# Optimization experiments

Measured on AMD Instinct MI355X. Metric: run time of the kernel, lower is better.

## Reference

```python
import jax, jax.numpy as jnp
import numpy as np

N_NODES = 25000
N_EDGES = 400000
HIDDEN = 256
NUM_FILTERS = 256
NUM_GAUSSIANS = 50
CUTOFF = 10.0


def ssp(x):
    # ShiftedSoftplus: softplus(x) - log(2)
    return jax.nn.softplus(x) - jnp.log(2.0).astype(x.dtype)


def setup_inputs() -> dict:
    key = jax.random.key(0)
    ks = jax.random.split(key, 12)
    s = 0.05
    return {
        "h": jax.random.normal(ks[0], (N_NODES, HIDDEN), dtype=jnp.float32),
        "pos": jax.random.uniform(ks[1], (N_NODES, 3), dtype=jnp.float32) * CUTOFF,
        "lin1_w": jax.random.normal(ks[2], (HIDDEN, NUM_FILTERS), dtype=jnp.float32) * s,
        "lin2_w": jax.random.normal(ks[3], (NUM_FILTERS, HIDDEN), dtype=jnp.float32) * s,
        "lin2_b": jnp.zeros((HIDDEN,), dtype=jnp.float32),
        "mlp_w1": jax.random.normal(ks[4], (NUM_GAUSSIANS, NUM_FILTERS), dtype=jnp.float32) * s,
        "mlp_b1": jnp.zeros((NUM_FILTERS,), dtype=jnp.float32),
        "mlp_w2": jax.random.normal(ks[5], (NUM_FILTERS, NUM_FILTERS), dtype=jnp.float32) * s,
        "mlp_b2": jnp.zeros((NUM_FILTERS,), dtype=jnp.float32),
        "lin_w": jax.random.normal(ks[6], (HIDDEN, HIDDEN), dtype=jnp.float32) * s,
        "lin_b": jnp.zeros((HIDDEN,), dtype=jnp.float32),
        "edge_index": jax.random.randint(ks[7], (2, N_EDGES), 0, N_NODES, dtype=jnp.int32),
    }


def reference(h, pos, lin1_w, lin2_w, lin2_b, mlp_w1, mlp_b1, mlp_w2, mlp_b2,
              lin_w, lin_b, edge_index):
    row, col = edge_index[0], edge_index[1]  # source, target (PyG convention)

    # edge distances
    diff = pos[row] - pos[col]                       # [E, 3]
    edge_weight = jnp.linalg.norm(diff, axis=-1)     # [E]

    # GaussianSmearing(0, cutoff, num_gaussians)
    offset = jnp.linspace(0.0, CUTOFF, NUM_GAUSSIANS, dtype=h.dtype)
    coeff = -0.5 / (offset[1] - offset[0]) ** 2
    edge_attr = jnp.exp(coeff * (edge_weight[:, None] - offset) ** 2)  # [E, G]

    # CFConv filter network * cosine cutoff
    W = ssp(edge_attr @ mlp_w1 + mlp_b1) @ mlp_w2 + mlp_b2             # [E, F]
    C = 0.5 * (jnp.cos(edge_weight * (jnp.pi / CUTOFF)) + 1.0)         # [E]
    W = W * C[:, None]

    # gather - multiply - scatter-add
    x = h @ lin1_w                                                     # [N, F] (no bias)
    msg = x[row] * W                                                   # [E, F]
    agg = jax.ops.segment_sum(msg, col, num_segments=N_NODES)          # [N, F]

    x = agg @ lin2_w + lin2_b
    x = ssp(x)
    h_update = x @ lin_w + lin_b                                       # [N, H]
    return (h_update, pos)
```

## Files before the change

### kernel.cpp

```cpp
#include <hip/hip_runtime.h>
#include <hip/hip_bf16.h>

#define N_NODES 25000
#define N_EDGES 400000
#define NTILES (N_EDGES / 32)

typedef __attribute__((ext_vector_type(8))) __bf16 bf16x8;
typedef __attribute__((ext_vector_type(4))) float f32x4;
typedef __attribute__((ext_vector_type(2))) unsigned uint32x2;

#define BAR() do {                                          \
    asm volatile("s_waitcnt lgkmcnt(0)" ::: "memory");      \
    __builtin_amdgcn_s_barrier();                           \
    asm volatile("" ::: "memory");                          \
} while (0)

static __device__ __forceinline__ unsigned short bfbits(float f) {
    __bf16 h = (__bf16)f;
    return __builtin_bit_cast(unsigned short, h);
}
static __device__ __forceinline__ float ssp_f(float x) {
    const float t = __builtin_amdgcn_exp2f(x * 1.44269504f);
    return 0.69314718f * (__builtin_amdgcn_logf(1.f + t) - 1.f);
}

template<int EPI, int OBF, int ABF>
__global__ __launch_bounds__(256, 2)
void node_gemm(const void* __restrict__ Av, const float* __restrict__ B,
               const float* __restrict__ bias, void* __restrict__ outv, int M)
{
    extern __shared__ char lds[];
    const int tid  = threadIdx.x;
    const int half = blockIdx.x & 1;
    const int jblk = half << 7;
    const int row0 = (blockIdx.x >> 1) << 7;

    {
        const int j   = tid & 127;
        const int k2b = (tid >> 7) << 6;
        for (int i = 0; i < 64; ++i) {
            const int k = (k2b + i) * 2;
            const float b0 = B[k * 256 + jblk + j];
            const float b1 = B[(k + 1) * 256 + jblk + j];
            const unsigned pack = (unsigned)bfbits(b0) | ((unsigned)bfbits(b1) << 16);
            *(unsigned*)(lds + ((j * 512 + k * 2) ^ ((j & 7) << 4))) = pack;
        }
    }
    __syncthreads();

    const int wave = tid >> 6;
    const int l    = tid & 63;
    const int lrow = l & 15;
    const int kg   = (l >> 4) << 3;

    f32x4 acc[8][2];
    const f32x4 z4 = {0.f, 0.f, 0.f, 0.f};
    #pragma unroll
    for (int m = 0; m < 8; ++m) { acc[m][0] = z4; acc[m][1] = z4; }

    #pragma unroll
    for (int ks = 0; ks < 8; ++ks) {
        const int k0 = (ks << 5) + kg;
        bf16x8 bfr[2];
        #pragma unroll
        for (int n = 0; n < 2; ++n) {
            const int jl = (wave << 5) + (n << 4) + lrow;
            bfr[n] = *(const bf16x8*)(lds + ((jl * 512 + k0 * 2) ^ ((jl & 7) << 4)));
        }
        #pragma unroll
        for (int m = 0; m < 8; ++m) {
            const int row = row0 + (m << 4) + lrow;
            bf16x8 af;
            if (row < M) {
                if (ABF) {
                    af = *(const bf16x8*)((const __bf16*)Av + row * 256 + k0);
                } else {
                    const float* ap = (const float*)Av + row * 256 + k0;
                    const f32x4 a0 = *(const f32x4*)(ap);
                    const f32x4 a1 = *(const f32x4*)(ap + 4);
                    #pragma unroll
                    for (int b = 0; b < 4; ++b) { af[b] = (__bf16)a0[b]; af[b + 4] = (__bf16)a1[b]; }
                }
            } else {
                #pragma unroll
                for (int b = 0; b < 8; ++b) af[b] = (__bf16)0.f;
            }
            acc[m][0] = __builtin_amdgcn_mfma_f32_16x16x32_bf16(af, bfr[0], acc[m][0], 0, 0, 0);
            acc[m][1] = __builtin_amdgcn_mfma_f32_16x16x32_bf16(af, bfr[1], acc[m][1], 0, 0, 0);
        }
    }

    #pragma unroll
    for (int m = 0; m < 8; ++m) {
        #pragma unroll
        for (int n = 0; n < 2; ++n) {
            const int j = jblk + (wave << 5) + (n << 4) + lrow;
            float bv = 0.f;
            if (EPI) bv = bias[j];
            #pragma unroll
            for (int r = 0; r < 4; ++r) {
                const int row = row0 + (m << 4) + ((l >> 4) << 2) + r;
                if (row < M) {
                    float v = acc[m][n][r] + bv;
                    if (EPI == 1) v = ssp_f(v);
                    if (OBF) ((unsigned short*)outv)[row * 256 + j] = bfbits(v);
                    else     ((float*)outv)[row * 256 + j] = v;
                }
            }
        }
    }
}

__global__ void hist_kernel(const int* __restrict__ ei, int* __restrict__ hist)
{
    const int i = blockIdx.x * 256 + threadIdx.x;
    if (i < N_EDGES) atomicAdd(&hist[ei[N_EDGES + i]], 1);
}

__global__ void scan_kernel(int* __restrict__ hist)
{
    __shared__ int part[1024];
    const int t  = threadIdx.x;
    const int CH = (N_NODES + 1023) / 1024;
    const int lo = t * CH;
    const int hi = (lo + CH < N_NODES) ? lo + CH : N_NODES;
    int s = 0;
    for (int i = lo; i < hi; ++i) s += hist[i];
    part[t] = s;
    __syncthreads();
    for (int off = 1; off < 1024; off <<= 1) {
        const int v = part[t];
        const int u = (t >= off) ? part[t - off] : 0;
        __syncthreads();
        part[t] = v + u;
        __syncthreads();
    }
    int base = (t == 0) ? 0 : part[t - 1];
    for (int i = lo; i < hi; ++i) { const int v = hist[i]; hist[i] = base; base += v; }
}

__global__ void scatter_meta(const int* __restrict__ ei, const float* __restrict__ pos,
                             int* __restrict__ hist, float4* __restrict__ meta,
                             float* __restrict__ out_pos)
{
    const int i = blockIdx.x * 256 + threadIdx.x;
    if (i >= N_EDGES) return;
    if (i < N_NODES * 3) out_pos[i] = pos[i];
    const int r = ei[i];
    const int c = ei[N_EDGES + i];
    const float dx = pos[r * 3 + 0] - pos[c * 3 + 0];
    const float dy = pos[r * 3 + 1] - pos[c * 3 + 1];
    const float dz = pos[r * 3 + 2] - pos[c * 3 + 2];
    const float d  = __fsqrt_rn(dx * dx + dy * dy + dz * dz);
    const float C  = 0.5f * (__cosf(d * 0.31415926535f) + 1.f);
    const int p = atomicAdd(&hist[c], 1);
    float4 m;
    m.x = d; m.y = C;
    m.z = __int_as_float(r); m.w = __int_as_float(c);
    meta[p] = m;
}

__global__ __launch_bounds__(256, 2)
void edge_kernel(const float4* __restrict__ meta,
                 const float* __restrict__ w1, const float* __restrict__ b1,
                 const float* __restrict__ w2, const float* __restrict__ b2,
                 const float* __restrict__ x, float* __restrict__ agg)
{
    extern __shared__ char lds[];
    char* w2t = lds;
    char* rb  = lds + 65536;
    int* colsm = (int*)(rb + 8192);

    const int tid   = threadIdx.x;
    const int wave  = tid >> 6;
    const int l     = tid & 63;
    const int lrow  = l & 15;
    const int g     = l >> 4;
    const int kg    = g << 3;
    const int half  = blockIdx.x & 1;
    const int jblk  = half << 7;
    const int group = blockIdx.x >> 1;

    {
        const int j   = tid & 127;
        const int k2b = (tid >> 7) << 6;
        for (int i = 0; i < 64; ++i) {
            const int k = (k2b + i) * 2;
            const float v0 = w2[k * 256 + jblk + j];
            const float v1 = w2[(k + 1) * 256 + jblk + j];
            const unsigned pack = (unsigned)bfbits(v0) | ((unsigned)bfbits(v1) << 16);
            *(unsigned*)(w2t + ((j * 512 + k * 2) ^ ((j & 7) << 4))) = pack;
        }
    }

    const float dlt    = 10.f / 49.f;
    const float coeff2 = (-0.5f / (dlt * dlt)) * 1.44269504f;
    bf16x8 w1f[4][2];
    #pragma unroll
    for (int n = 0; n < 4; ++n)
        #pragma unroll
        for (int ks = 0; ks < 2; ++ks) {
            bf16x8 v;
            #pragma unroll
            for (int b = 0; b < 8; ++b) {
                const int k = (ks << 5) + kg + b;
                const int j = (wave << 6) + (n << 4) + lrow;
                v[b] = (k < 50) ? (__bf16)w1[k * 256 + j] : (__bf16)0.f;
            }
            w1f[n][ks] = v;
        }
    float b1v[4], b2v[2];
    #pragma unroll
    for (int n = 0; n < 4; ++n) b1v[n] = b1[(wave << 6) + (n << 4) + lrow];
    #pragma unroll
    for (int n = 0; n < 2; ++n) b2v[n] = b2[jblk + (wave << 5) + (n << 4) + lrow];

    BAR();

    const f32x4 z4 = {0.f, 0.f, 0.f, 0.f};
    const int CH = (NTILES + 255) / 256;
    const int t0 = group * CH;
    int t1 = t0 + CH; if (t1 > NTILES) t1 = NTILES;

    const int ge  = tid >> 3;
    const int gkb = (tid & 7) << 3;

    int   rprev  = -1;
    float rs     = 0.f;
    int   rfirst = 1;
    float* aj    = agg + jblk + (tid & 127);

    for (int t = t0; t < t1; ++t) {
        const float4 mv = meta[(t << 5) + (l & 31)];
        const float d  = mv.x;
        const float Cc = mv.y;
        const int   r  = __float_as_int(mv.z);
        const int   c  = __float_as_int(mv.w);

        float xv[2][2][4];
        #pragma unroll
        for (int m = 0; m < 2; ++m)
            #pragma unroll
            for (int r4 = 0; r4 < 4; ++r4) {
                const int e  = (m << 4) + (g << 2) + r4;
                const int re = __shfl(r, e, 64);
                #pragma unroll
                for (int n = 0; n < 2; ++n) {
                    const int jloc = (wave << 5) + (n << 4) + lrow;
                    xv[m][n][r4] = x[re * 256 + jblk + jloc];
                }
            }

        const float gd = __shfl(d, ge, 64);
        bf16x8 gv;
        #pragma unroll
        for (int b = 0; b < 8; ++b) {
            const int k = gkb + b;
            float gval = 0.f;
            if (k < 50) {
                const float u = gd - (float)k * dlt;
                gval = __builtin_amdgcn_exp2f(coeff2 * u * u);
            }
            gv[b] = (__bf16)gval;
        }

        BAR();
        *(bf16x8*)(rb + ((ge * 128 + (gkb << 1)) ^ ((ge & 7) << 4))) = gv;
        BAR();

        bf16x8 af[2][2];
        #pragma unroll
        for (int m = 0; m < 2; ++m) {
            const int e = (m << 4) + lrow;
            #pragma unroll
            for (int ks = 0; ks < 2; ++ks)
                af[m][ks] = *(const bf16x8*)(rb + ((e * 128 + ((ks << 5) + kg) * 2) ^ ((e & 7) << 4)));
        }
        f32x4 acc1[2][4];
        #pragma unroll
        for (int m = 0; m < 2; ++m)
            #pragma unroll
            for (int n = 0; n < 4; ++n) acc1[m][n] = z4;
        #pragma unroll
        for (int ks = 0; ks < 2; ++ks)
            #pragma unroll
            for (int m = 0; m < 2; ++m)
                #pragma unroll
                for (int n = 0; n < 4; ++n)
                    acc1[m][n] = __builtin_amdgcn_mfma_f32_16x16x32_bf16(af[m][ks], w1f[n][ks], acc1[m][n], 0, 0, 0);
        BAR();

        #pragma unroll
        for (int m = 0; m < 2; ++m)
            #pragma unroll
            for (int n = 0; n < 4; ++n)
                #pragma unroll
                for (int r4 = 0; r4 < 4; ++r4) {
                    const int e = (m << 4) + (g << 2) + r4;
                    const int k = (wave << 6) + (n << 4) + lrow;
                    const float v = ssp_f(acc1[m][n][r4] + b1v[n]);
                    *(__bf16*)(rb + ((e * 512 + k * 2) ^ ((e & 7) << 4))) = (__bf16)v;
                }
        BAR();

        f32x4 acc2[2][2];
        #pragma unroll
        for (int m = 0; m < 2; ++m) { acc2[m][0] = z4; acc2[m][1] = z4; }
        #pragma unroll
        for (int ks = 0; ks < 8; ++ks) {
            const int k0 = (ks << 5) + kg;
            bf16x8 bfr[2];
            #pragma unroll
            for (int n = 0; n < 2; ++n) {
                const int jl = (wave << 5) + (n << 4) + lrow;
                bfr[n] = *(const bf16x8*)(w2t + ((jl * 512 + k0 * 2) ^ ((jl & 7) << 4)));
            }
            #pragma unroll
            for (int m = 0; m < 2; ++m) {
                const int e = (m << 4) + lrow;
                const bf16x8 a = *(const bf16x8*)(rb + ((e * 512 + k0 * 2) ^ ((e & 7) << 4)));
                #pragma unroll
                for (int n = 0; n < 2; ++n)
                    acc2[m][n] = __builtin_amdgcn_mfma_f32_16x16x32_bf16(a, bfr[n], acc2[m][n], 0, 0, 0);
            }
        }
        BAR();

        #pragma unroll
        for (int m = 0; m < 2; ++m) {
            const int base_e = (m << 4) + (g << 2);
            #pragma unroll
            for (int n = 0; n < 2; ++n) {
                const int jloc = (wave << 5) + (n << 4) + lrow;
                float vv[4];
                #pragma unroll
                for (int r4 = 0; r4 < 4; ++r4) {
                    const int e  = base_e + r4;
                    const float Ce = __shfl(Cc, e, 64);
                    vv[r4] = (acc2[m][n][r4] + b2v[n]) * Ce * xv[m][n][r4];
                }
                uint32x2 pk;
                pk[0] = (unsigned)bfbits(vv[0]) | ((unsigned)bfbits(vv[1]) << 16);
                pk[1] = (unsigned)bfbits(vv[2]) | ((unsigned)bfbits(vv[3]) << 16);
                *(uint32x2*)(rb + ((jloc * 64 + (base_e << 1)) ^ ((jloc & 7) << 4))) = pk;
            }
        }
        if (tid < 32) colsm[tid] = c;
        BAR();

        if (tid < 128) {
            const int j = tid;
            const bf16x8 q0 = *(const bf16x8*)(rb + ((j * 64 +  0) ^ ((j & 7) << 4)));
            const bf16x8 q1 = *(const bf16x8*)(rb + ((j * 64 + 16) ^ ((j & 7) << 4)));
            const bf16x8 q2 = *(const bf16x8*)(rb + ((j * 64 + 32) ^ ((j & 7) << 4)));
            const bf16x8 q3 = *(const bf16x8*)(rb + ((j * 64 + 48) ^ ((j & 7) << 4)));
            #pragma unroll
            for (int e = 0; e < 32; ++e) {
                const float v = (float)(e < 8 ? q0[e] : e < 16 ? q1[e - 8] :
                                        e < 24 ? q2[e - 16] : q3[e - 24]);
                const int ce = colsm[e];
                if (ce != rprev) {
                    if (rprev >= 0) {
                        if (rfirst) { atomicAdd(aj + rprev * 256, rs); rfirst = 0; }
                        else        { aj[rprev * 256] = rs; }
                    }
                    rs = 0.f; rprev = ce;
                }
                rs += v;
            }
        }
    }
    if (tid < 128 && rprev >= 0) atomicAdd(aj + rprev * 256, rs);
}

extern "C" void kernel_launch(void* const* d_in, const int* in_sizes, int n_in,
                              void* d_out, int out_size, void* d_ws, size_t ws_size,
                              hipStream_t stream)
{
    const float* h      = (const float*)d_in[0];
    const float* pos    = (const float*)d_in[1];
    const float* lin1_w = (const float*)d_in[2];
    const float* lin2_w = (const float*)d_in[3];
    const float* lin2_b = (const float*)d_in[4];
    const float* mlp_w1 = (const float*)d_in[5];
    const float* mlp_b1 = (const float*)d_in[6];
    const float* mlp_w2 = (const float*)d_in[7];
    const float* mlp_b2 = (const float*)d_in[8];
    const float* lin_w  = (const float*)d_in[9];
    const float* lin_b  = (const float*)d_in[10];
    const int*   ei     = (const int*)d_in[11];
    float* out = (float*)d_out;

    float*  x    = (float*)d_ws;
    float*  agg  = (float*)((char*)d_ws + 25600000);
    float4* meta = (float4*)((char*)d_ws + 51200000);
    int*    hist = (int*)((char*)d_ws + 57600000);
    unsigned short* xb = (unsigned short*)d_ws;

    (void)hipFuncSetAttribute((const void*)edge_kernel,
                              hipFuncAttributeMaxDynamicSharedMemorySize, 81920);
    (void)hipFuncSetAttribute((const void*)node_gemm<0, 0, 0>,
                              hipFuncAttributeMaxDynamicSharedMemorySize, 65536);
    (void)hipFuncSetAttribute((const void*)node_gemm<1, 1, 0>,
                              hipFuncAttributeMaxDynamicSharedMemorySize, 65536);
    (void)hipFuncSetAttribute((const void*)node_gemm<2, 0, 1>,
                              hipFuncAttributeMaxDynamicSharedMemorySize, 65536);

    (void)hipMemsetAsync(agg, 0, (size_t)N_NODES * 256 * sizeof(float), stream);
    (void)hipMemsetAsync(hist, 0, (size_t)N_NODES * sizeof(int), stream);

    const dim3 blk(256);
    const int mt = (N_NODES + 127) / 128;
    const int eb = (N_EDGES + 255) / 256;

    node_gemm<0, 0, 0><<<dim3(mt * 2), blk, 65536, stream>>>(h, lin1_w, nullptr, x, N_NODES);

    hist_kernel<<<dim3(eb), blk, 0, stream>>>(ei, hist);
    scan_kernel<<<dim3(1), dim3(1024), 0, stream>>>(hist);
    scatter_meta<<<dim3(eb), blk, 0, stream>>>(ei, pos, hist, meta, out + N_NODES * 256);

    edge_kernel<<<dim3(512), blk, 81920, stream>>>(meta, mlp_w1, mlp_b1,
                                                   mlp_w2, mlp_b2, x, agg);

    node_gemm<1, 1, 0><<<dim3(mt * 2), blk, 65536, stream>>>(agg, lin2_w, lin2_b, xb, N_NODES);
    node_gemm<2, 0, 1><<<dim3(mt * 2), blk, 65536, stream>>>(xb, lin_w, lin_b, out, N_NODES);
}
```

Baseline: 447.5 us.

## Use FP8 for edge filter second GEMM and split LDS buffers to drop barriers

New measurement: 642.9 us. 43.7% more time.

```diff
diff --git a/kernel.cpp b/kernel.cpp
--- a/kernel.cpp
+++ b/kernel.cpp
@@ -8,6 +8,7 @@
 typedef __attribute__((ext_vector_type(8))) __bf16 bf16x8;
 typedef __attribute__((ext_vector_type(4))) float f32x4;
 typedef __attribute__((ext_vector_type(2))) unsigned uint32x2;
+typedef long long ll64;
 
 #define BAR() do {                                          \
     asm volatile("s_waitcnt lgkmcnt(0)" ::: "memory");      \
@@ -18,6 +19,14 @@
 static __device__ __forceinline__ unsigned short bfbits(float f) {
     __bf16 h = (__bf16)f;
     return __builtin_bit_cast(unsigned short, h);
+}
+static __device__ __forceinline__ unsigned f8pack4(float a, float b, float c, float d) {
+    int p = __builtin_amdgcn_cvt_pk_fp8_f32(a, b, 0, false);
+    p = __builtin_amdgcn_cvt_pk_fp8_f32(c, d, p, true);
+    return (unsigned)p;
+}
+static __device__ __forceinline__ unsigned char f8bits(float f) {
+    return (unsigned char)(__builtin_amdgcn_cvt_pk_fp8_f32(f, f, 0, false) & 0xff);
 }
 static __device__ __forceinline__ float ssp_f(float x) {
     const float t = __builtin_amdgcn_exp2f(x * 1.44269504f);
@@ -160,7 +169,7 @@
     meta[p] = m;
 }
 
-__global__ __launch_bounds__(256, 2)
+__global__ __launch_bounds__(256, 3)
 void edge_kernel(const float4* __restrict__ meta,
                  const float* __restrict__ w1, const float* __restrict__ b1,
                  const float* __restrict__ w2, const float* __restrict__ b2,
@@ -168,8 +177,10 @@
 {
     extern __shared__ char lds[];
     char* w2t = lds;
-    char* rb  = lds + 65536;
-    int* colsm = (int*)(rb + 8192);
+    char* tb  = lds + 32768;
+    char* gs  = lds + 40960;
+    char* ms  = lds + 45056;
+    int* colsm = (int*)(lds + 53248);
 
     const int tid   = threadIdx.x;
     const int wave  = tid >> 6;
@@ -182,14 +193,15 @@
     const int group = blockIdx.x >> 1;
 
     {
-        const int j   = tid & 127;
-        const int k2b = (tid >> 7) << 6;
-        for (int i = 0; i < 64; ++i) {
-            const int k = (k2b + i) * 2;
-            const float v0 = w2[k * 256 + jblk + j];
+        const int j  = tid & 127;
+        const int kq = (tid >> 7) << 7;
+        for (int i = 0; i < 32; ++i) {
+            const int k = kq + i * 4;
+            const float v0 = w2[(k + 0) * 256 + jblk + j];
             const float v1 = w2[(k + 1) * 256 + jblk + j];
-            const unsigned pack = (unsigned)bfbits(v0) | ((unsigned)bfbits(v1) << 16);
-            *(unsigned*)(w2t + ((j * 512 + k * 2) ^ ((j & 7) << 4))) = pack;
+            const float v2 = w2[(k + 2) * 256 + jblk + j];
+            const float v3 = w2[(k + 3) * 256 + jblk + j];
+            *(unsigned*)(w2t + ((j * 256 + k) ^ ((j & 15) << 3))) = f8pack4(v0, v1, v2, v3);
         }
     }
 
@@ -263,9 +275,7 @@
             }
             gv[b] = (__bf16)gval;
         }
-
-        BAR();
-        *(bf16x8*)(rb + ((ge * 128 + (gkb << 1)) ^ ((ge & 7) << 4))) = gv;
+        *(bf16x8*)(gs + ((ge * 128 + (gkb << 1)) ^ ((ge & 7) << 4))) = gv;
         BAR();
 
         bf16x8 af[2][2];
@@ -274,7 +284,7 @@
             const int e = (m << 4) + lrow;
             #pragma unroll
             for (int ks = 0; ks < 2; ++ks)
-                af[m][ks] = *(const bf16x8*)(rb + ((e * 128 + ((ks << 5) + kg) * 2) ^ ((e & 7) << 4)));
+                af[m][ks] = *(const bf16x8*)(gs + ((e * 128 + ((ks << 5) + kg) * 2) ^ ((e & 7) << 4)));
         }
         f32x4 acc1[2][4];
         #pragma unroll
@@ -288,7 +298,6 @@
                 #pragma unroll
                 for (int n = 0; n < 4; ++n)
                     acc1[m][n] = __builtin_amdgcn_mfma_f32_16x16x32_bf16(af[m][ks], w1f[n][ks], acc1[m][n], 0, 0, 0);
-        BAR();
 
         #pragma unroll
         for (int m = 0; m < 2; ++m)
@@ -299,7 +308,7 @@
                     const int e = (m << 4) + (g << 2) + r4;
                     const int k = (wave << 6) + (n << 4) + lrow;
                     const float v = ssp_f(acc1[m][n][r4] + b1v[n]);
-                    *(__bf16*)(rb + ((e * 512 + k * 2) ^ ((e & 7) << 4))) = (__bf16)v;
+                    *(unsigned char*)(tb + ((e * 256 + k) ^ ((e & 15) << 3))) = f8bits(v);
                 }
         BAR();
 
@@ -309,22 +318,21 @@
         #pragma unroll
         for (int ks = 0; ks < 8; ++ks) {
             const int k0 = (ks << 5) + kg;
-            bf16x8 bfr[2];
+            ll64 bfr[2];
             #pragma unroll
             for (int n = 0; n < 2; ++n) {
                 const int jl = (wave << 5) + (n << 4) + lrow;
-                bfr[n] = *(const bf16x8*)(w2t + ((jl * 512 + k0 * 2) ^ ((jl & 7) << 4)));
+                bfr[n] = *(const ll64*)(w2t + ((jl * 256 + k0) ^ ((jl & 15) << 3)));
             }
             #pragma unroll
             for (int m = 0; m < 2; ++m) {
                 const int e = (m << 4) + lrow;
-                const bf16x8 a = *(const bf16x8*)(rb + ((e * 512 + k0 * 2) ^ ((e & 7) << 4)));
+                const ll64 a = *(const ll64*)(tb + ((e * 256 + k0) ^ ((e & 15) << 3)));
                 #pragma unroll
                 for (int n = 0; n < 2; ++n)
-                    acc2[m][n] = __builtin_amdgcn_mfma_f32_16x16x32_bf16(a, bfr[n], acc2[m][n], 0, 0, 0);
-            }
-        }
-        BAR();
+                    acc2[m][n] = __builtin_amdgcn_mfma_f32_16x16x32_fp8_fp8(a, bfr[n], acc2[m][n], 0, 0, 0);
+            }
+        }
 
         #pragma unroll
         for (int m = 0; m < 2; ++m) {
@@ -342,7 +350,7 @@
                 uint32x2 pk;
                 pk[0] = (unsigned)bfbits(vv[0]) | ((unsigned)bfbits(vv[1]) << 16);
                 pk[1] = (unsigned)bfbits(vv[2]) | ((unsigned)bfbits(vv[3]) << 16);
-                *(uint32x2*)(rb + ((jloc * 64 + (base_e << 1)) ^ ((jloc & 7) << 4))) = pk;
+                *(uint32x2*)(ms + ((jloc * 64 + (base_e << 1)) ^ ((jloc & 7) << 4))) = pk;
             }
         }
         if (tid < 32) colsm[tid] = c;
@@ -350,10 +358,10 @@
 
         if (tid < 128) {
             const int j = tid;
-            const bf16x8 q0 = *(const bf16x8*)(rb + ((j * 64 +  0) ^ ((j & 7) << 4)));
-            const bf16x8 q1 = *(const bf16x8*)(rb + ((j * 64 + 16) ^ ((j & 7) << 4)));
-            const bf16x8 q2 = *(const bf16x8*)(rb + ((j * 64 + 32) ^ ((j & 7) << 4)));
-            const bf16x8 q3 = *(const bf16x8*)(rb + ((j * 64 + 48) ^ ((j & 7) << 4)));
+            const bf16x8 q0 = *(const bf16x8*)(ms + ((j * 64 +  0) ^ ((j & 7) << 4)));
+            const bf16x8 q1 = *(const bf16x8*)(ms + ((j * 64 + 16) ^ ((j & 7) << 4)));
+            const bf16x8 q2 = *(const bf16x8*)(ms + ((j * 64 + 32) ^ ((j & 7) << 4)));
+            const bf16x8 q3 = *(const bf16x8*)(ms + ((j * 64 + 48) ^ ((j & 7) << 4)));
             #pragma unroll
             for (int e = 0; e < 32; ++e) {
                 const float v = (float)(e < 8 ? q0[e] : e < 16 ? q1[e - 8] :
@@ -398,7 +406,7 @@
     unsigned short* xb = (unsigned short*)d_ws;
 
     (void)hipFuncSetAttribute((const void*)edge_kernel,
-                              hipFuncAttributeMaxDynamicSharedMemorySize, 81920);
+                              hipFuncAttributeMaxDynamicSharedMemorySize, 53376);
     (void)hipFuncSetAttribute((const void*)node_gemm<0, 0, 0>,
                               hipFuncAttributeMaxDynamicSharedMemorySize, 65536);
     (void)hipFuncSetAttribute((const void*)node_gemm<1, 1, 0>,
@@ -419,7 +427,7 @@
     scan_kernel<<<dim3(1), dim3(1024), 0, stream>>>(hist);
     scatter_meta<<<dim3(eb), blk, 0, stream>>>(ei, pos, hist, meta, out + N_NODES * 256);
 
-    edge_kernel<<<dim3(512), blk, 81920, stream>>>(meta, mlp_w1, mlp_b1,
+    edge_kernel<<<dim3(512), blk, 53376, stream>>>(meta, mlp_w1, mlp_b1,
                                                    mlp_w2, mlp_b2, x, agg);
 
     node_gemm<1, 1, 0><<<dim3(mt * 2), blk, 65536, stream>>>(agg, lin2_w, lin2_b, xb, N_NODES);
```
